# Optimization experiments

Measured on AMD Instinct MI355X. Metric: run time of the kernel, lower is better.

## Reference

```python
import jax, jax.numpy as jnp
import numpy as np

DEPTH = 6
N_LEAF = 2 ** DEPTH          # 64
GATE_COUNT = N_LEAF - 1      # 63
IN_F = 512
OUT_F = 512
BATCH = 1024


def setup_inputs() -> dict:
    key = jax.random.key(0)
    k1, k2, k3 = jax.random.split(key, 3)
    x = jax.random.normal(k1, (BATCH, IN_F), dtype=jnp.float32)
    gw = jax.random.normal(k2, (IN_F, GATE_COUNT), dtype=jnp.float32)
    gb = jnp.zeros((GATE_COUNT,), dtype=jnp.float32)
    pw = jax.random.normal(k3, (OUT_F, IN_F, N_LEAF), dtype=jnp.float32)
    pb = jnp.zeros((OUT_F, N_LEAF), dtype=jnp.float32)
    return {"x": x, "gw": gw, "gb": gb, "pw": pw, "pb": pb}


def _leaf_probs(x, gw, gb, depth):
    # gatings: sigmoid(x @ gw + gb), shape [B, gate_count]
    g = jax.nn.sigmoid(x @ gw + gb)
    B = x.shape[0]
    dens = jnp.ones((B, 1), dtype=x.dtype)  # root density
    offset = 0
    for d in range(depth):
        n = 2 ** d
        gp = g[:, offset:offset + n]                    # parent gatings [B, n]
        # left child multiplies by g, right child by (1 - g), interleaved
        pair = jnp.stack([gp, 1.0 - gp], axis=-1).reshape(B, 2 * n)
        dens = jnp.repeat(dens, 2, axis=1) * pair        # [B, 2n]
        offset += n
    return dens  # [B, n_leaf]


def reference(x, gw, gb, pw, pb):
    leaf = _leaf_probs(x, gw, gb, DEPTH)                 # [B, L]
    # per-leaf linear projections, then mix with leaf probabilities
    y = jnp.einsum('bi,oil->bol', x, pw)                 # [B, O, L]
    out = jnp.einsum('bol,bl->bo', y, leaf) + leaf @ pb.T
    return out
```

## Files before the change

### kernel.cpp

```cpp
#include <hip/hip_runtime.h>
#include <hip/hip_bf16.h>

#define TDEPTH 6
#define NLEAF 64
#define NGATE 63
#define INF 512
#define OUTF 512
#define BATCH 1024

#define BM 256
#define BN 64
#define THREADS 256

typedef __attribute__((ext_vector_type(4)))  float f32x4;
typedef __attribute__((ext_vector_type(16))) float f32x16;
typedef __attribute__((ext_vector_type(8)))  __bf16 bf16x8;

__device__ __forceinline__ bf16x8 pack8(f32x4 a, f32x4 b) {
  bf16x8 w;
  w[0] = (__bf16)a[0]; w[1] = (__bf16)a[1];
  w[2] = (__bf16)a[2]; w[3] = (__bf16)a[3];
  w[4] = (__bf16)b[0]; w[5] = (__bf16)b[1];
  w[6] = (__bf16)b[2]; w[7] = (__bf16)b[3];
  return w;
}

__global__ __launch_bounds__(256) void prep_kernel(
    const float* __restrict__ x, const float* __restrict__ gw,
    const float* __restrict__ gb, const float* __restrict__ pw,
    float* __restrict__ leaf, __bf16* __restrict__ pwb) {
  const int tid = threadIdx.x;
  if (blockIdx.x < 256) {
    const int wid = tid >> 6, lane = tid & 63;
    const int b = blockIdx.x * 4 + wid;
    __shared__ float g[4][NLEAF];
    if (lane < NGATE) {
      const float* xr = x + (size_t)b * INF;
      float a0 = 0.f, a1 = 0.f, a2 = 0.f, a3 = 0.f;
      #pragma unroll 4
      for (int i = 0; i < INF; i += 4) {
        a0 += xr[i + 0] * gw[(i + 0) * NGATE + lane];
        a1 += xr[i + 1] * gw[(i + 1) * NGATE + lane];
        a2 += xr[i + 2] * gw[(i + 2) * NGATE + lane];
        a3 += xr[i + 3] * gw[(i + 3) * NGATE + lane];
      }
      float t = (a0 + a1) + (a2 + a3) + gb[lane];
      g[wid][lane] = 1.0f / (1.0f + __expf(-t));
    }
    __syncthreads();
    float p = 1.0f;
    #pragma unroll
    for (int d = 0; d < TDEPTH; d++) {
      int prefix = lane >> (TDEPTH - 1 - d);
      int node = (1 << d) - 1 + (prefix >> 1);
      float gv = g[wid][node];
      p *= (prefix & 1) ? (1.0f - gv) : gv;
    }
    leaf[(size_t)b * NLEAF + lane] = p;
  } else {
    const unsigned G = (blockIdx.x - 256) * 256 + tid;
    const unsigned o = G >> 12, rem = G & 4095;
    const unsigned ipair = rem >> 4, p = rem & 15;
    const unsigned g = p ^ (o & 15);
    const unsigned i = ipair * 2 + (g >> 3), kg = g & 7;
    const float* src = pw + (((size_t)o * INF + i) * NLEAF + kg * 8);
    f32x4 a = *(const f32x4*)src, b = *(const f32x4*)(src + 4);
    *(bf16x8*)((char*)pwb + (((size_t)o << 16) + (ipair << 8) + (p << 4))) =
        pack8(a, b);
  }
}

__device__ __forceinline__ void gload_lds16(const void* g, void* l) {
  __builtin_amdgcn_global_load_lds(
      (const __attribute__((address_space(1))) void*)g,
      (__attribute__((address_space(3))) void*)l, 16, 0, 0);
}

template <int S>
__global__ __launch_bounds__(THREADS, 2) void gemm_kernel(
    const __bf16* __restrict__ pwb, const float* __restrict__ pb,
    const float* __restrict__ x, const float* __restrict__ leaf,
    float* __restrict__ partial) {
  constexpr int NSTEP = 256 / S;
  constexpr int NPL = 512 / S;
  __shared__ __align__(16) __bf16 Bsm[3][BN * 128];
  __shared__ __align__(16) __bf16 xsm[NPL][BM];

  const int tid = threadIdx.x, lane = tid & 63, w = tid >> 6;
  const int lo = lane & 31, half = lane >> 5;

  const int nwg = 4 * 8 * S;
  const int L = (blockIdx.x & 7) * (nwg / 8) + (blockIdx.x >> 3);
  const int mb = L & 3;
  const int rest = L >> 2;
  const int nb = rest & 7, s = rest >> 3;
  const int m0 = mb * BM, n0 = nb * BN;
  const int ip0 = s * NSTEP;
  const int cs = s * NPL;

  f32x4 lf[2][4][2];
  #pragma unroll
  for (int mt = 0; mt < 2; mt++) {
    const float* lr =
        leaf + (size_t)(m0 + w * 64 + mt * 32 + lo) * NLEAF + half * 8;
    #pragma unroll
    for (int t4 = 0; t4 < 4; t4++) {
      lf[mt][t4][0] = *(const f32x4*)(lr + t4 * 16);
      lf[mt][t4][1] = *(const f32x4*)(lr + t4 * 16 + 4);
    }
  }

  {
    const float* src = x + (size_t)(m0 + tid) * INF + cs;
    #pragma unroll
    for (int c4 = 0; c4 < NPL / 4; c4++) {
      f32x4 v = *(const f32x4*)(src + c4 * 4);
      #pragma unroll
      for (int j = 0; j < 4; j++) xsm[c4 * 4 + j][tid] = (__bf16)v[j];
    }
  }

  size_t pwoff[4];
  #pragma unroll
  for (int j = 0; j < 4; j++) {
    int r = j * 16 + w * 4 + (lane >> 4);
    pwoff[j] = ((size_t)(n0 + r) << 16) + ((unsigned)(lane & 15) << 4);
  }
  const char* pwc = (const char*)pwb;

  auto stage = [&](char* dstb, int t) {
    const char* srcb = pwc + ((size_t)(ip0 + t) << 8);
    #pragma unroll
    for (int j = 0; j < 4; j++)
      gload_lds16(srcb + pwoff[j], dstb + j * 4096 + w * 1024);
  };

  f32x16 acc00 = (f32x16)(0.f), acc01 = (f32x16)(0.f);
  f32x16 acc10 = (f32x16)(0.f), acc11 = (f32x16)(0.f);
  const unsigned swz = (unsigned)(lo & 15) << 4;

  auto do_step = [&](const char* bufc, int t) {
    const float xv00 = (float)xsm[2 * t][w * 64 + lo];
    const float xv01 = (float)xsm[2 * t + 1][w * 64 + lo];
    const float xv10 = (float)xsm[2 * t][w * 64 + 32 + lo];
    const float xv11 = (float)xsm[2 * t + 1][w * 64 + 32 + lo];
    #pragma unroll
    for (int pl = 0; pl < 2; pl++) {
      const float x0 = pl ? xv01 : xv00;
      const float x1 = pl ? xv11 : xv10;
      #pragma unroll
      for (int t4 = 0; t4 < 4; t4++) {
        const unsigned kb = ((unsigned)(pl * 128 + t4 * 32 + half * 16)) ^ swz;
        bf16x8 bf0 = *(const bf16x8*)(bufc + lo * 256 + kb);
        bf16x8 bf1 = *(const bf16x8*)(bufc + (32 + lo) * 256 + kb);
        f32x4 p0a = lf[0][t4][0] * x0, p0b = lf[0][t4][1] * x0;
        f32x4 p1a = lf[1][t4][0] * x1, p1b = lf[1][t4][1] * x1;
        bf16x8 a0 = pack8(p0a, p0b);
        bf16x8 a1 = pack8(p1a, p1b);
        acc00 = __builtin_amdgcn_mfma_f32_32x32x16_bf16(a0, bf0, acc00, 0, 0, 0);
        acc01 = __builtin_amdgcn_mfma_f32_32x32x16_bf16(a0, bf1, acc01, 0, 0, 0);
        acc10 = __builtin_amdgcn_mfma_f32_32x32x16_bf16(a1, bf0, acc10, 0, 0, 0);
        acc11 = __builtin_amdgcn_mfma_f32_32x32x16_bf16(a1, bf1, acc11, 0, 0, 0);
      }
    }
  };

  char* bA = (char*)&Bsm[0][0];
  char* bB = (char*)&Bsm[1][0];
  char* bC = (char*)&Bsm[2][0];

  stage(bA, 0);
  stage(bB, 1);
  __builtin_amdgcn_sched_barrier(0);
  asm volatile("s_waitcnt vmcnt(0) lgkmcnt(0)" ::: "memory");
  __builtin_amdgcn_s_barrier();
  __builtin_amdgcn_sched_barrier(0);

  for (int t = 0; t < NSTEP - 2; ++t) {
    stage(bC, t + 2);
    do_step(bA, t);
    __builtin_amdgcn_sched_barrier(0);
    asm volatile("s_waitcnt vmcnt(4) lgkmcnt(0)" ::: "memory");
    __builtin_amdgcn_s_barrier();
    __builtin_amdgcn_sched_barrier(0);
    char* tmp = bA; bA = bB; bB = bC; bC = tmp;
  }
  do_step(bA, NSTEP - 2);
  __builtin_amdgcn_sched_barrier(0);
  asm volatile("s_waitcnt vmcnt(0) lgkmcnt(0)" ::: "memory");
  __builtin_amdgcn_s_barrier();
  __builtin_amdgcn_sched_barrier(0);
  do_step(bB, NSTEP - 1);

  if (s == S - 1) {
    #pragma unroll
    for (int t4 = 0; t4 < 4; t4++) {
      bf16x8 a0 = pack8(lf[0][t4][0], lf[0][t4][1]);
      bf16x8 a1 = pack8(lf[1][t4][0], lf[1][t4][1]);
      #pragma unroll
      for (int nt = 0; nt < 2; nt++) {
        const float* pr =
            pb + (size_t)(n0 + nt * 32 + lo) * NLEAF + t4 * 16 + half * 8;
        f32x4 c0 = *(const f32x4*)pr, c1 = *(const f32x4*)(pr + 4);
        bf16x8 bb = pack8(c0, c1);
        if (nt == 0) {
          acc00 = __builtin_amdgcn_mfma_f32_32x32x16_bf16(a0, bb, acc00, 0, 0, 0);
          acc10 = __builtin_amdgcn_mfma_f32_32x32x16_bf16(a1, bb, acc10, 0, 0, 0);
        } else {
          acc01 = __builtin_amdgcn_mfma_f32_32x32x16_bf16(a0, bb, acc01, 0, 0, 0);
          acc11 = __builtin_amdgcn_mfma_f32_32x32x16_bf16(a1, bb, acc11, 0, 0, 0);
        }
      }
    }
  }

  #pragma unroll
  for (int mt = 0; mt < 2; mt++) {
    float* dst =
        partial + ((size_t)s * BATCH + m0 + w * 64 + mt * 32) * OUTF + n0;
    #pragma unroll
    for (int e = 0; e < 16; e++) {
      int row = (e & 3) + 8 * (e >> 2) + 4 * half;
      if (mt == 0) {
        dst[(size_t)row * OUTF + lo] = acc00[e];
        dst[(size_t)row * OUTF + 32 + lo] = acc01[e];
      } else {
        dst[(size_t)row * OUTF + lo] = acc10[e];
        dst[(size_t)row * OUTF + 32 + lo] = acc11[e];
      }
    }
  }
}

template <int S>
__global__ __launch_bounds__(256) void reduce_kernel(
    const float* __restrict__ partial, float* __restrict__ out) {
  size_t e = ((size_t)blockIdx.x * 256 + threadIdx.x) * 4;
  f32x4 sum = (f32x4){0.f, 0.f, 0.f, 0.f};
  #pragma unroll
  for (int s = 0; s < S; s++)
    sum += *(const f32x4*)(partial + (size_t)s * BATCH * OUTF + e);
  *(f32x4*)(out + e) = sum;
}

extern "C" void kernel_launch(void* const* d_in, const int* in_sizes, int n_in,
                              void* d_out, int out_size, void* d_ws, size_t ws_size,
                              hipStream_t stream) {
  const float* x  = (const float*)d_in[0];
  const float* gw = (const float*)d_in[1];
  const float* gb = (const float*)d_in[2];
  const float* pw = (const float*)d_in[3];
  const float* pb = (const float*)d_in[4];
  float* out = (float*)d_out;

  float*  leaf    = (float*)d_ws;
  __bf16* pwb     = (__bf16*)((char*)d_ws + (1 << 20));
  float*  partial = (float*)((char*)d_ws + (33ull << 20));

  prep_kernel<<<256 + 8192, 256, 0, stream>>>(x, gw, gb, pw, leaf, pwb);

  const size_t need16 = (33ull << 20) + (size_t)16 * BATCH * OUTF * 4;
  if (ws_size >= need16) {
    gemm_kernel<16><<<4 * 8 * 16, THREADS, 0, stream>>>(pwb, pb, x, leaf, partial);
    reduce_kernel<16><<<(BATCH * OUTF) / (256 * 4), 256, 0, stream>>>(partial, out);
  } else {
    gemm_kernel<8><<<4 * 8 * 8, THREADS, 0, stream>>>(pwb, pb, x, leaf, partial);
    reduce_kernel<8><<<(BATCH * OUTF) / (256 * 4), 256, 0, stream>>>(partial, out);
  }
}
```

Measured before the change: 70.48 us.

## Retile GEMM to 128-row blocks with 128 threads and contiguous per-tile weight layout

The prep kernel now writes the bf16 weight copy so that each (column block, input feature) tile is one contiguous 8 KB chunk, which lets the staging loads use plain linear addresses. The GEMM block shrinks to 128 rows and 2 waves, and each step covers one input feature instead of two, giving 1024 workgroups in place of 512. The workspace-size fallback is dropped and split-K is fixed at 16. More, smaller blocks should fill the CUs better, but every weight tile is now re-read by twice as many M blocks and each step carries more barrier overhead per MFMA.

```diff
diff --git a/kernel.cpp b/kernel.cpp
--- a/kernel.cpp
+++ b/kernel.cpp
@@ -8,9 +8,11 @@
 #define OUTF 512
 #define BATCH 1024
 
-#define BM 256
+#define BM 128
 #define BN 64
-#define THREADS 256
+#define SPLITK 16
+#define THREADS 128
+#define NPL 32
 
 typedef __attribute__((ext_vector_type(4)))  float f32x4;
 typedef __attribute__((ext_vector_type(16))) float f32x16;
@@ -58,15 +60,17 @@
     }
     leaf[(size_t)b * NLEAF + lane] = p;
   } else {
-    const unsigned G = (blockIdx.x - 256) * 256 + tid;
-    const unsigned o = G >> 12, rem = G & 4095;
-    const unsigned ipair = rem >> 4, p = rem & 15;
-    const unsigned g = p ^ (o & 15);
-    const unsigned i = ipair * 2 + (g >> 3), kg = g & 7;
-    const float* src = pw + (((size_t)o * INF + i) * NLEAF + kg * 8);
+    const unsigned Q = (blockIdx.x - 256) * 256 + tid;
+    const unsigned tile = Q >> 9;
+    const unsigned nb = tile >> 9, i = tile & 511;
+    const unsigned q = Q & 511;
+    const unsigned r = ((q >> 7) << 3) + ((q >> 4) & 7);
+    const unsigned v = (q & 15) ^ (r & 15);
+    const unsigned o = nb * 64 + ((v >> 3) << 5) + r;
+    const unsigned kg = v & 7;
+    const float* src = pw + ((size_t)o * INF + i) * NLEAF + kg * 8;
     f32x4 a = *(const f32x4*)src, b = *(const f32x4*)(src + 4);
-    *(bf16x8*)((char*)pwb + (((size_t)o << 16) + (ipair << 8) + (p << 4))) =
-        pack8(a, b);
+    *(bf16x8*)((char*)pwb + (size_t)Q * 16) = pack8(a, b);
   }
 }
 
@@ -76,26 +80,21 @@
       (__attribute__((address_space(3))) void*)l, 16, 0, 0);
 }
 
-template <int S>
 __global__ __launch_bounds__(THREADS, 2) void gemm_kernel(
     const __bf16* __restrict__ pwb, const float* __restrict__ pb,
     const float* __restrict__ x, const float* __restrict__ leaf,
     float* __restrict__ partial) {
-  constexpr int NSTEP = 256 / S;
-  constexpr int NPL = 512 / S;
-  __shared__ __align__(16) __bf16 Bsm[3][BN * 128];
+  __shared__ __align__(16) __bf16 Bsm[3][32 * 128];
   __shared__ __align__(16) __bf16 xsm[NPL][BM];
 
   const int tid = threadIdx.x, lane = tid & 63, w = tid >> 6;
   const int lo = lane & 31, half = lane >> 5;
 
-  const int nwg = 4 * 8 * S;
-  const int L = (blockIdx.x & 7) * (nwg / 8) + (blockIdx.x >> 3);
-  const int mb = L & 3;
-  const int rest = L >> 2;
+  const int L = (blockIdx.x & 7) * 128 + (blockIdx.x >> 3);
+  const int mb = L & 7;
+  const int rest = L >> 3;
   const int nb = rest & 7, s = rest >> 3;
   const int m0 = mb * BM, n0 = nb * BN;
-  const int ip0 = s * NSTEP;
   const int cs = s * NPL;
 
   f32x4 lf[2][4][2];
@@ -120,19 +119,14 @@
     }
   }
 
-  size_t pwoff[4];
-  #pragma unroll
-  for (int j = 0; j < 4; j++) {
-    int r = j * 16 + w * 4 + (lane >> 4);
-    pwoff[j] = ((size_t)(n0 + r) << 16) + ((unsigned)(lane & 15) << 4);
-  }
   const char* pwc = (const char*)pwb;
+  const size_t tbase = (size_t)(nb * 512 + cs) << 13;
 
   auto stage = [&](char* dstb, int t) {
-    const char* srcb = pwc + ((size_t)(ip0 + t) << 8);
+    const char* srcb = pwc + tbase + ((size_t)t << 13);
     #pragma unroll
     for (int j = 0; j < 4; j++)
-      gload_lds16(srcb + pwoff[j], dstb + j * 4096 + w * 1024);
+      gload_lds16(srcb + j * 2048 + tid * 16, dstb + j * 2048 + w * 1024);
   };
 
   f32x16 acc00 = (f32x16)(0.f), acc01 = (f32x16)(0.f);
@@ -140,28 +134,22 @@
   const unsigned swz = (unsigned)(lo & 15) << 4;
 
   auto do_step = [&](const char* bufc, int t) {
-    const float xv00 = (float)xsm[2 * t][w * 64 + lo];
-    const float xv01 = (float)xsm[2 * t + 1][w * 64 + lo];
-    const float xv10 = (float)xsm[2 * t][w * 64 + 32 + lo];
-    const float xv11 = (float)xsm[2 * t + 1][w * 64 + 32 + lo];
-    #pragma unroll
-    for (int pl = 0; pl < 2; pl++) {
-      const float x0 = pl ? xv01 : xv00;
-      const float x1 = pl ? xv11 : xv10;
-      #pragma unroll
-      for (int t4 = 0; t4 < 4; t4++) {
-        const unsigned kb = ((unsigned)(pl * 128 + t4 * 32 + half * 16)) ^ swz;
-        bf16x8 bf0 = *(const bf16x8*)(bufc + lo * 256 + kb);
-        bf16x8 bf1 = *(const bf16x8*)(bufc + (32 + lo) * 256 + kb);
-        f32x4 p0a = lf[0][t4][0] * x0, p0b = lf[0][t4][1] * x0;
-        f32x4 p1a = lf[1][t4][0] * x1, p1b = lf[1][t4][1] * x1;
-        bf16x8 a0 = pack8(p0a, p0b);
-        bf16x8 a1 = pack8(p1a, p1b);
-        acc00 = __builtin_amdgcn_mfma_f32_32x32x16_bf16(a0, bf0, acc00, 0, 0, 0);
-        acc01 = __builtin_amdgcn_mfma_f32_32x32x16_bf16(a0, bf1, acc01, 0, 0, 0);
-        acc10 = __builtin_amdgcn_mfma_f32_32x32x16_bf16(a1, bf0, acc10, 0, 0, 0);
-        acc11 = __builtin_amdgcn_mfma_f32_32x32x16_bf16(a1, bf1, acc11, 0, 0, 0);
-      }
+    const float xv0 = (float)xsm[t][w * 64 + lo];
+    const float xv1 = (float)xsm[t][w * 64 + 32 + lo];
+    #pragma unroll
+    for (int t4 = 0; t4 < 4; t4++) {
+      const unsigned kb0 = ((unsigned)(t4 * 32 + half * 16)) ^ swz;
+      const unsigned kb1 = ((unsigned)(128 + t4 * 32 + half * 16)) ^ swz;
+      bf16x8 bf0 = *(const bf16x8*)(bufc + lo * 256 + kb0);
+      bf16x8 bf1 = *(const bf16x8*)(bufc + lo * 256 + kb1);
+      f32x4 p0a = lf[0][t4][0] * xv0, p0b = lf[0][t4][1] * xv0;
+      f32x4 p1a = lf[1][t4][0] * xv1, p1b = lf[1][t4][1] * xv1;
+      bf16x8 a0 = pack8(p0a, p0b);
+      bf16x8 a1 = pack8(p1a, p1b);
+      acc00 = __builtin_amdgcn_mfma_f32_32x32x16_bf16(a0, bf0, acc00, 0, 0, 0);
+      acc01 = __builtin_amdgcn_mfma_f32_32x32x16_bf16(a0, bf1, acc01, 0, 0, 0);
+      acc10 = __builtin_amdgcn_mfma_f32_32x32x16_bf16(a1, bf0, acc10, 0, 0, 0);
+      acc11 = __builtin_amdgcn_mfma_f32_32x32x16_bf16(a1, bf1, acc11, 0, 0, 0);
     }
   };
 
@@ -172,11 +160,11 @@
   stage(bA, 0);
   stage(bB, 1);
   __builtin_amdgcn_sched_barrier(0);
-  asm volatile("s_waitcnt vmcnt(0) lgkmcnt(0)" ::: "memory");
+  asm volatile("s_waitcnt vmcnt(4) lgkmcnt(0)" ::: "memory");
   __builtin_amdgcn_s_barrier();
   __builtin_amdgcn_sched_barrier(0);
 
-  for (int t = 0; t < NSTEP - 2; ++t) {
+  for (int t = 0; t < NPL - 2; ++t) {
     stage(bC, t + 2);
     do_step(bA, t);
     __builtin_amdgcn_sched_barrier(0);
@@ -185,14 +173,14 @@
     __builtin_amdgcn_sched_barrier(0);
     char* tmp = bA; bA = bB; bB = bC; bC = tmp;
   }
-  do_step(bA, NSTEP - 2);
+  do_step(bA, NPL - 2);
   __builtin_amdgcn_sched_barrier(0);
   asm volatile("s_waitcnt vmcnt(0) lgkmcnt(0)" ::: "memory");
   __builtin_amdgcn_s_barrier();
   __builtin_amdgcn_sched_barrier(0);
-  do_step(bB, NSTEP - 1);
-
-  if (s == S - 1) {
+  do_step(bB, NPL - 1);
+
+  if (s == SPLITK - 1) {
     #pragma unroll
     for (int t4 = 0; t4 < 4; t4++) {
       bf16x8 a0 = pack8(lf[0][t4][0], lf[0][t4][1]);
@@ -232,13 +220,12 @@
   }
 }
 
-template <int S>
 __global__ __launch_bounds__(256) void reduce_kernel(
     const float* __restrict__ partial, float* __restrict__ out) {
   size_t e = ((size_t)blockIdx.x * 256 + threadIdx.x) * 4;
   f32x4 sum = (f32x4){0.f, 0.f, 0.f, 0.f};
   #pragma unroll
-  for (int s = 0; s < S; s++)
+  for (int s = 0; s < SPLITK; s++)
     sum += *(const f32x4*)(partial + (size_t)s * BATCH * OUTF + e);
   *(f32x4*)(out + e) = sum;
 }
@@ -258,13 +245,6 @@
   float*  partial = (float*)((char*)d_ws + (33ull << 20));
 
   prep_kernel<<<256 + 8192, 256, 0, stream>>>(x, gw, gb, pw, leaf, pwb);
-
-  const size_t need16 = (33ull << 20) + (size_t)16 * BATCH * OUTF * 4;
-  if (ws_size >= need16) {
-    gemm_kernel<16><<<4 * 8 * 16, THREADS, 0, stream>>>(pwb, pb, x, leaf, partial);
-    reduce_kernel<16><<<(BATCH * OUTF) / (256 * 4), 256, 0, stream>>>(partial, out);
-  } else {
-    gemm_kernel<8><<<4 * 8 * 8, THREADS, 0, stream>>>(pwb, pb, x, leaf, partial);
-    reduce_kernel<8><<<(BATCH * OUTF) / (256 * 4), 256, 0, stream>>>(partial, out);
-  }
-}
+  gemm_kernel<<<8 * 8 * SPLITK, THREADS, 0, stream>>>(pwb, pb, x, leaf, partial);
+  reduce_kernel<<<(BATCH * OUTF) / (256 * 4), 256, 0, stream>>>(partial, out);
+}
```

Result: slower. 75.39 us (+7.0%).
